# Performance work log

Hardware: AMD Instinct MI355X
Metric: run time of the kernel (lower is better)

The kernel has to match this reference:

```python
import jax, jax.numpy as jnp
import numpy as np

B, S, E, H = 4, 2048, 1024, 8
D = E // H  # head_dim = 128


def setup_inputs() -> dict:
    key = jax.random.key(0)
    ks = jax.random.split(key, 7)
    scale = 1.0 / np.sqrt(D)
    return {
        "sequences": jax.random.normal(ks[0], (B, S, E), dtype=jnp.float32),
        # per-head Linear weights, torch layout [out, in] stacked over heads
        "Wq": jax.random.normal(ks[1], (H, D, D), dtype=jnp.float32) * scale,
        "Wk": jax.random.normal(ks[2], (H, D, D), dtype=jnp.float32) * scale,
        "Wv": jax.random.normal(ks[3], (H, D, D), dtype=jnp.float32) * scale,
        "bq": jax.random.normal(ks[4], (H, D), dtype=jnp.float32) * scale,
        "bk": jax.random.normal(ks[5], (H, D), dtype=jnp.float32) * scale,
        "bv": jax.random.normal(ks[6], (H, D), dtype=jnp.float32) * scale,
    }


def reference(sequences, Wq, Wk, Wv, bq, bk, bv):
    # split feature dim into heads: [B,S,H,D]
    xh = sequences.reshape(B, S, H, D)
    # torch Linear: y = x @ W.T + b  ->  contract input dim d with W[h, o, d]
    q = jnp.einsum("bshd,hod->bsho", xh, Wq) + bq
    k = jnp.einsum("bshd,hod->bsho", xh, Wk) + bk
    v = jnp.einsum("bshd,hod->bsho", xh, Wv) + bv
    # NOTE: original scales by 1/sqrt(num_heads), not 1/sqrt(head_dim)
    scores = jnp.einsum("bshd,bthd->bhst", q, k) / jnp.sqrt(jnp.float32(H))
    attn = jax.nn.softmax(scores, axis=-1)  # [B,H,S,S]
    out = jnp.einsum("bhst,bthd->bshd", attn, v)
    # hstack over heads == reshape back to [B,S,E]
    return out.reshape(B, S, E)
```

## Files before the change

### kernel.cpp

```cpp
#include <hip/hip_runtime.h>
#include <hip/hip_bf16.h>

#define B_ 4
#define S_ 2048
#define E_ 1024
#define H_ 8
#define D_ 128

using f16x8 = __attribute__((ext_vector_type(8))) _Float16;
using f32x4 = __attribute__((ext_vector_type(4))) float;

__device__ __forceinline__ ushort f2h_bits(float f) {
    union { _Float16 h; ushort u; } cv; cv.h = (_Float16)f; return cv.u;
}
__device__ __forceinline__ float max3f(float a, float b, float c) {
    return fmaxf(fmaxf(a, b), c);
}
__device__ __forceinline__ f16x8 pack8(const float* __restrict__ p) {
    float4 f0 = *(const float4*)p;
    float4 f1 = *(const float4*)(p + 4);
    f16x8 r;
    r[0] = (_Float16)f0.x; r[1] = (_Float16)f0.y;
    r[2] = (_Float16)f0.z; r[3] = (_Float16)f0.w;
    r[4] = (_Float16)f1.x; r[5] = (_Float16)f1.y;
    r[6] = (_Float16)f1.z; r[7] = (_Float16)f1.w;
    return r;
}

__device__ __forceinline__ void gll16(const ushort* g, ushort* l) {
    __builtin_amdgcn_global_load_lds(
        (const __attribute__((address_space(1))) unsigned int*)g,
        (__attribute__((address_space(3))) unsigned int*)l, 16, 0, 0);
}

__global__ __launch_bounds__(256) void kv_proj(
    const float* __restrict__ seq,
    const float* __restrict__ Wk, const float* __restrict__ Wv,
    const float* __restrict__ bk, const float* __restrict__ bv,
    ushort* __restrict__ ko, ushort* __restrict__ vo)
{
    constexpr int TS = 136;
    __shared__ ushort Tk[128 * TS];
    __shared__ ushort Tv[128 * TS];
    const int m0 = blockIdx.x * 128, h = blockIdx.y;
    const int tid = threadIdx.x, lane = tid & 63, w = tid >> 6;
    const int l16 = lane & 15, quad = lane >> 4;

    f16x8 a[2][4];
    #pragma unroll
    for (int mt = 0; mt < 2; ++mt)
        #pragma unroll
        for (int ks = 0; ks < 4; ++ks)
            a[mt][ks] = pack8(&seq[(size_t)(m0 + w * 32 + mt * 16 + l16) * E_
                                   + h * D_ + ks * 32 + quad * 8]);

    {
        const float* W = Wk + (size_t)h * D_ * D_;
        f32x4 acc[2][8];
        #pragma unroll
        for (int mt = 0; mt < 2; ++mt)
            #pragma unroll
            for (int nt = 0; nt < 8; ++nt) { f32x4 z = {0.f,0.f,0.f,0.f}; acc[mt][nt] = z; }
        #pragma unroll
        for (int ks = 0; ks < 4; ++ks)
            #pragma unroll
            for (int nt = 0; nt < 8; ++nt) {
                f16x8 bfr = pack8(&W[(size_t)(nt * 16 + l16) * D_ + ks * 32 + quad * 8]);
                #pragma unroll
                for (int mt = 0; mt < 2; ++mt)
                    acc[mt][nt] = __builtin_amdgcn_mfma_f32_16x16x32_f16(
                        a[mt][ks], bfr, acc[mt][nt], 0, 0, 0);
            }
        #pragma unroll
        for (int nt = 0; nt < 8; ++nt) {
            int o = nt * 16 + l16;
            float bias = bk[h * D_ + o];
            #pragma unroll
            for (int mt = 0; mt < 2; ++mt)
                #pragma unroll
                for (int r = 0; r < 4; ++r) {
                    int row = w * 32 + mt * 16 + quad * 4 + r;
                    Tk[row * TS + (o ^ (quad << 3))] = f2h_bits(acc[mt][nt][r] + bias);
                }
        }
    }
    {
        const float* W = Wv + (size_t)h * D_ * D_;
        f32x4 acc[2][8];
        #pragma unroll
        for (int mt = 0; mt < 2; ++mt)
            #pragma unroll
            for (int nt = 0; nt < 8; ++nt) { f32x4 z = {0.f,0.f,0.f,0.f}; acc[mt][nt] = z; }
        #pragma unroll
        for (int ks = 0; ks < 4; ++ks)
            #pragma unroll
            for (int nt = 0; nt < 8; ++nt) {
                f16x8 bfr = pack8(&W[(size_t)(nt * 16 + l16) * D_ + ks * 32 + quad * 8]);
                #pragma unroll
                for (int mt = 0; mt < 2; ++mt)
                    acc[mt][nt] = __builtin_amdgcn_mfma_f32_16x16x32_f16(
                        a[mt][ks], bfr, acc[mt][nt], 0, 0, 0);
            }
        #pragma unroll
        for (int nt = 0; nt < 8; ++nt) {
            int o = nt * 16 + l16;
            float bias = bv[h * D_ + o];
            #pragma unroll
            for (int mt = 0; mt < 2; ++mt)
                #pragma unroll
                for (int r = 0; r < 4; ++r) {
                    int row = w * 32 + mt * 16 + quad * 4 + r;
                    Tv[o * TS + row] = f2h_bits(acc[mt][nt][r] + bias);
                }
        }
    }
    __syncthreads();

    #pragma unroll
    for (int i = 0; i < 8; ++i) {
        int idx = tid + i * 256;
        int row = idx >> 4, c8 = (idx & 15) * 8;
        int lk = c8 ^ ((row & 7) << 3);
        uint4 dk = *(uint4*)&Tk[row * TS + (lk ^ (((row >> 2) & 3) << 3))];
        int m = m0 + row, bi = m >> 11, s = m & (S_ - 1);
        *(uint4*)&ko[(((size_t)bi * H_ + h) * S_ + s) * D_ + c8] = dk;
        int cc = idx & 15;
        int s2v = (row ^ (row >> 2)) & 3;
        uint4 dv = *(uint4*)&Tv[row * TS + (((cc & 12) | ((cc & 3) ^ s2v)) << 3)];
        int mg = m0 + cc * 8, bv_i = mg >> 11, s0 = mg & (S_ - 1);
        *(uint4*)&vo[(((size_t)bv_i * H_ + h) * D_ + row) * S_ + s0] = dv;
    }
}

__global__ __launch_bounds__(512, 4) void attn(
    const float* __restrict__ seq, const float* __restrict__ Wq,
    const float* __restrict__ bq,
    const ushort* __restrict__ kg, const ushort* __restrict__ vtg,
    float* __restrict__ out)
{
    constexpr int NT = S_ / 32;
    __shared__ alignas(16) ushort smem[20480];
    ushort* const Kb0 = smem;
    ushort* const Kb1 = smem + 4096;
    ushort* const Vb0 = smem + 8192;
    ushort* const Vb1 = smem + 12288;
    ushort* const Pbuf = smem + 16384;
    ushort* const Qs = smem;

    const int L = blockIdx.x + 16 * blockIdx.y + 128 * blockIdx.z;
    const int c = L & 7, t = L >> 3;
    const int g = c * 4 + (t & 3);
    const int h = g & 7, bi = g >> 3;
    const int m0 = (t >> 2) * 128;

    const int bh = bi * H_ + h;
    const int tid = threadIdx.x, lane = tid & 63, w = tid >> 6;
    const int l16 = lane & 15, quad = lane >> 4;
    const int swz = l16 & 7;
    const int s2 = (l16 ^ (l16 >> 2)) & 3;
    const ushort* kbase = kg + (size_t)bh * S_ * D_;
    const ushort* vbase = vtg + (size_t)bh * D_ * S_;
    const float qscale = 0.35355339059327373f * 1.4426950408889634f;

    {
        f16x8 xa[4];
        #pragma unroll
        for (int ks = 0; ks < 4; ++ks)
            xa[ks] = pack8(&seq[((size_t)bi * S_ + m0 + w * 16 + l16) * E_
                                + h * D_ + ks * 32 + quad * 8]);
        f32x4 qacc[8];
        #pragma unroll
        for (int nt = 0; nt < 8; ++nt) { f32x4 z = {0.f,0.f,0.f,0.f}; qacc[nt] = z; }
        const float* W = Wq + (size_t)h * D_ * D_;
        #pragma unroll
        for (int ks = 0; ks < 4; ++ks)
            #pragma unroll
            for (int nt = 0; nt < 8; ++nt) {
                f16x8 bfr = pack8(&W[(size_t)(nt * 16 + l16) * D_ + ks * 32 + quad * 8]);
                qacc[nt] = __builtin_amdgcn_mfma_f32_16x16x32_f16(
                    xa[ks], bfr, qacc[nt], 0, 0, 0);
            }
        #pragma unroll
        for (int nt = 0; nt < 8; ++nt) {
            int o = nt * 16 + l16;
            float bias = bq[h * D_ + o];
            #pragma unroll
            for (int r = 0; r < 4; ++r) {
                int row = w * 16 + quad * 4 + r;
                Qs[row * 128 + (o ^ (quad << 3))] =
                    f2h_bits((qacc[nt][r] + bias) * qscale);
            }
        }
    }
    __syncthreads();

    f16x8 qf[4];
    #pragma unroll
    for (int ks = 0; ks < 4; ++ks)
        qf[ks] = *(const f16x8*)&Qs[(w * 16 + l16) * 128
                                    + ks * 32 + ((quad ^ (l16 >> 2)) << 3)];
    __syncthreads();

    gll16(kbase + w * 512 + lane * 8, Kb0 + w * 512);
    gll16(vbase + (size_t)(w * 16 + (lane >> 2)) * S_ + (lane & 3) * 8,
          Vb0 + w * 512);

    f32x4 o_acc[8];
    #pragma unroll
    for (int nt = 0; nt < 8; ++nt) { f32x4 z = {0.f,0.f,0.f,0.f}; o_acc[nt] = z; }
    float m_prev = -1e30f, l_lane = 0.f;

    __syncthreads();

    ushort* const prow = &Pbuf[(w * 16 + l16) * 32];

    #pragma unroll 2
    for (int j = 0; j < NT; ++j) {
        const int cur = j & 1;
        const ushort* KL = cur ? Kb1 : Kb0;
        const ushort* VL = cur ? Vb1 : Vb0;

        if (j + 1 < NT) {
            const ushort* kt = kbase + (size_t)(j + 1) * 32 * 128;
            const ushort* vt = vbase + (j + 1) * 32;
            ushort* kd = cur ? Kb0 : Kb1;
            ushort* vd = cur ? Vb0 : Vb1;
            gll16(kt + w * 512 + lane * 8, kd + w * 512);
            gll16(vt + (size_t)(w * 16 + (lane >> 2)) * S_ + (lane & 3) * 8,
                  vd + w * 512);
        }

        f32x4 sacc[2];
        #pragma unroll
        for (int nt = 0; nt < 2; ++nt) { f32x4 z = {0.f,0.f,0.f,0.f}; sacc[nt] = z; }
        __builtin_amdgcn_s_setprio(1);
        #pragma unroll
        for (int ks = 0; ks < 4; ++ks)
            #pragma unroll
            for (int nt = 0; nt < 2; ++nt) {
                f16x8 kf = *(const f16x8*)&KL[(nt * 16 + l16) * 128
                                              + (((ks * 4 + quad) ^ swz) << 3)];
                sacc[nt] = __builtin_amdgcn_mfma_f32_16x16x32_f16(
                    kf, qf[ks], sacc[nt], 0, 0, 0);
            }
        __builtin_amdgcn_s_setprio(0);

        {
            float v0 = max3f(sacc[0][0], sacc[0][1], sacc[0][2]);
            float v1 = max3f(sacc[0][3], sacc[1][0], sacc[1][1]);
            float mx = max3f(v0, v1, fmaxf(sacc[1][2], sacc[1][3]));
            mx = fmaxf(mx, __shfl_xor(mx, 16));
            mx = fmaxf(mx, __shfl_xor(mx, 32));
            if (__any(mx > m_prev + 8.0f)) {
                float mnew  = fmaxf(m_prev, mx);
                float alpha = exp2f(m_prev - mnew);
                #pragma unroll
                for (int nt = 0; nt < 8; ++nt)
                    #pragma unroll
                    for (int r = 0; r < 4; ++r) o_acc[nt][r] *= alpha;
                l_lane *= alpha;
                m_prev = mnew;
            }
            #pragma unroll
            for (int nt = 0; nt < 2; ++nt) {
                float e0 = exp2f(sacc[nt][0] - m_prev);
                float e1 = exp2f(sacc[nt][1] - m_prev);
                float e2 = exp2f(sacc[nt][2] - m_prev);
                float e3 = exp2f(sacc[nt][3] - m_prev);
                auto p01 = __builtin_amdgcn_cvt_pkrtz(e0, e1);
                auto p23 = __builtin_amdgcn_cvt_pkrtz(e2, e3);
                int G = 2 * nt + (quad >> 1);
                *(uint2*)&prow[((G ^ s2) << 3) + ((quad & 1) << 2)] =
                    make_uint2(__builtin_bit_cast(uint, p01),
                               __builtin_bit_cast(uint, p23));
                l_lane += (float)p01[0] + (float)p01[1] + (float)p23[0] + (float)p23[1];
            }
        }

        __builtin_amdgcn_s_setprio(1);
        {
            f16x8 pb = *(const f16x8*)&prow[((quad ^ s2) << 3)];
            #pragma unroll
            for (int nt = 0; nt < 8; ++nt) {
                f16x8 vf = *(const f16x8*)&VL[(nt * 16 + l16) * 32
                                              + ((quad ^ s2) << 3)];
                o_acc[nt] = __builtin_amdgcn_mfma_f32_16x16x32_f16(
                    vf, pb, o_acc[nt], 0, 0, 0);
            }
        }
        __builtin_amdgcn_s_setprio(0);

        __syncthreads();
    }

    {
        float l = l_lane;
        l += __shfl_xor(l, 16);
        l += __shfl_xor(l, 32);
        float rinv = 1.0f / l;
        const int q = m0 + w * 16 + l16;
        #pragma unroll
        for (int nt = 0; nt < 8; ++nt) {
            float4 o;
            o.x = o_acc[nt][0] * rinv;
            o.y = o_acc[nt][1] * rinv;
            o.z = o_acc[nt][2] * rinv;
            o.w = o_acc[nt][3] * rinv;
            *(float4*)&out[((size_t)bi * S_ + q) * E_ + h * D_ + nt * 16 + quad * 4] = o;
        }
    }
}

extern "C" void kernel_launch(void* const* d_in, const int* in_sizes, int n_in,
                              void* d_out, int out_size, void* d_ws, size_t ws_size,
                              hipStream_t stream) {
    const float* seq = (const float*)d_in[0];
    const float* Wq  = (const float*)d_in[1];
    const float* Wk  = (const float*)d_in[2];
    const float* Wv  = (const float*)d_in[3];
    const float* bq  = (const float*)d_in[4];
    const float* bk  = (const float*)d_in[5];
    const float* bv  = (const float*)d_in[6];

    const size_t per = (size_t)B_ * H_ * S_ * D_;
    if (ws_size < 2 * per * sizeof(ushort)) return;
    ushort* kws  = (ushort*)d_ws;
    ushort* vtws = kws + per;

    kv_proj<<<dim3(B_ * S_ / 128, H_), 256, 0, stream>>>(
        seq, Wk, Wv, bk, bv, kws, vtws);
    attn<<<dim3(16, 8, 4), 512, 0, stream>>>(
        seq, Wq, bq, kws, vtws, (float*)d_out);
}
```

Before: 252.5 us.

## Load V fragments directly from global into registers instead of LDS

Removes the double-buffered LDS staging of the V tile in the attention loop. Each wave now loads its V MFMA operands directly from global memory into registers every iteration, and the projection kernel stores V unswizzled to match. This cuts LDS footprint and traffic, which could help occupancy. In exchange each wave re-reads the same V data from L2/global with less latency hiding, since there is no cross-iteration prefetch.

Result: slower. 408.7 us (+61.9%).

```diff
diff --git a/kernel.cpp b/kernel.cpp
--- a/kernel.cpp
+++ b/kernel.cpp
@@ -124,10 +124,8 @@
         uint4 dk = *(uint4*)&Tk[row * TS + (lk ^ (((row >> 2) & 3) << 3))];
         int m = m0 + row, bi = m >> 11, s = m & (S_ - 1);
         *(uint4*)&ko[(((size_t)bi * H_ + h) * S_ + s) * D_ + c8] = dk;
-        int cc = idx & 15;
-        int s2v = (row ^ (row >> 2)) & 3;
-        uint4 dv = *(uint4*)&Tv[row * TS + (((cc & 12) | ((cc & 3) ^ s2v)) << 3)];
-        int mg = m0 + cc * 8, bv_i = mg >> 11, s0 = mg & (S_ - 1);
+        uint4 dv = *(uint4*)&Tv[row * TS + c8];
+        int mg = m0 + c8, bv_i = mg >> 11, s0 = mg & (S_ - 1);
         *(uint4*)&vo[(((size_t)bv_i * H_ + h) * D_ + row) * S_ + s0] = dv;
     }
 }
@@ -139,12 +137,10 @@
     float* __restrict__ out)
 {
     constexpr int NT = S_ / 32;
-    __shared__ alignas(16) ushort smem[20480];
+    __shared__ alignas(16) ushort smem[16384];
     ushort* const Kb0 = smem;
     ushort* const Kb1 = smem + 4096;
-    ushort* const Vb0 = smem + 8192;
-    ushort* const Vb1 = smem + 12288;
-    ushort* const Pbuf = smem + 16384;
+    ushort* const Pbuf = smem + 8192;
     ushort* const Qs = smem;
 
     const int L = blockIdx.x + 16 * blockIdx.y + 128 * blockIdx.z;
@@ -202,8 +198,11 @@
     __syncthreads();
 
     gll16(kbase + w * 512 + lane * 8, Kb0 + w * 512);
-    gll16(vbase + (size_t)(w * 16 + (lane >> 2)) * S_ + (lane & 3) * 8,
-          Vb0 + w * 512);
+
+    int voffs[8];
+    #pragma unroll
+    for (int nt = 0; nt < 8; ++nt)
+        voffs[nt] = (nt * 16 + l16) * S_ + quad * 8;
 
     f32x4 o_acc[8];
     #pragma unroll
@@ -218,17 +217,17 @@
     for (int j = 0; j < NT; ++j) {
         const int cur = j & 1;
         const ushort* KL = cur ? Kb1 : Kb0;
-        const ushort* VL = cur ? Vb1 : Vb0;
 
         if (j + 1 < NT) {
-            const ushort* kt = kbase + (size_t)(j + 1) * 32 * 128;
-            const ushort* vt = vbase + (j + 1) * 32;
-            ushort* kd = cur ? Kb0 : Kb1;
-            ushort* vd = cur ? Vb0 : Vb1;
-            gll16(kt + w * 512 + lane * 8, kd + w * 512);
-            gll16(vt + (size_t)(w * 16 + (lane >> 2)) * S_ + (lane & 3) * 8,
-                  vd + w * 512);
-        }
+            gll16(kbase + (j + 1) * 4096 + w * 512 + lane * 8,
+                  (cur ? Kb0 : Kb1) + w * 512);
+        }
+
+        const ushort* vb = vbase + j * 32;
+        f16x8 vr[8];
+        #pragma unroll
+        for (int nt = 0; nt < 8; ++nt)
+            vr[nt] = *(const f16x8*)(vb + voffs[nt]);
 
         f32x4 sacc[2];
         #pragma unroll
@@ -281,12 +280,9 @@
         {
             f16x8 pb = *(const f16x8*)&prow[((quad ^ s2) << 3)];
             #pragma unroll
-            for (int nt = 0; nt < 8; ++nt) {
-                f16x8 vf = *(const f16x8*)&VL[(nt * 16 + l16) * 32
-                                              + ((quad ^ s2) << 3)];
+            for (int nt = 0; nt < 8; ++nt)
                 o_acc[nt] = __builtin_amdgcn_mfma_f32_16x16x32_f16(
-                    vf, pb, o_acc[nt], 0, 0, 0);
-            }
+                    vr[nt], pb, o_acc[nt], 0, 0, 0);
         }
         __builtin_amdgcn_s_setprio(0);
 
```
